# Kernel optimization log

Hardware: AMD Instinct MI355X
Metric: run time of the kernel (lower is better)

The kernel has to match this reference:

```python
import jax, jax.numpy as jnp
import numpy as np

B, D, T = 16384, 1024, 128  # batch, embed_dim, num_degradation_types
V, L = 4, 3                 # variants per sample, degradations per variant


def setup_inputs() -> dict:
    key = jax.random.key(0)
    k1, k2, k3, k4 = jax.random.split(key, 4)
    clean_embeddings = jax.random.normal(k1, (B, D), dtype=jnp.float32)
    W = jax.random.normal(k2, (T, D), dtype=jnp.float32) * (1.0 / np.sqrt(D))
    b = jnp.zeros((T,), dtype=jnp.float32)
    deg_indices = jax.random.randint(k3, (B, V, L), 0, T, dtype=jnp.int32)
    deg_mask = jax.random.randint(k4, (B, V, L), 0, 2, dtype=jnp.int32)
    return {"clean_embeddings": clean_embeddings, "W": W, "b": b,
            "deg_indices": deg_indices, "deg_mask": deg_mask}


def reference(clean_embeddings, W, b, deg_indices, deg_mask):
    # Linear + softmax: [B, T]
    logits = jnp.einsum("bd,td->bt", clean_embeddings, W) + b
    probs = jax.nn.softmax(logits, axis=-1)
    # Gather probs at each (batch, label) pair: [B, V*L] -> [B, V, L]
    flat_idx = deg_indices.reshape(B, V * L)
    gathered = jnp.take_along_axis(probs, flat_idx, axis=1).reshape(B, V, L)
    # Masked sum over all labels of a sample, divided by max(num_variants, 1)=V
    per_sample = (gathered * deg_mask.astype(probs.dtype)).sum(axis=(1, 2)) / V
    return per_sample.sum() / B
```

## Files before the change

### kernel.cpp

```cpp
#include <hip/hip_runtime.h>

#define B_SIZE 16384
#define D_DIM  1024
#define T_DIM  128
#define VLn    12
#define BM     64
#define BKF    64
#define NCHUNK 16
#define NTHR   512
#define GRID   (B_SIZE / BM)
#define ACHB   16384
#define BCHB   16384
#define PAIRB  (ACHB + BCHB)
#define SLSTR  132

typedef _Float16 half8  __attribute__((ext_vector_type(8)));
typedef __fp16   fp16x2 __attribute__((ext_vector_type(2)));
typedef float    f32x4  __attribute__((ext_vector_type(4)));

union Pack16 { fp16x2 h[4]; uint4 u; half8 v; };
union Frag   { uint4 u; half8 h; };

__device__ __forceinline__ uint4 pack8u(float4 v0, float4 v1) {
    Pack16 un;
    un.h[0] = __builtin_amdgcn_cvt_pkrtz(v0.x, v0.y);
    un.h[1] = __builtin_amdgcn_cvt_pkrtz(v0.z, v0.w);
    un.h[2] = __builtin_amdgcn_cvt_pkrtz(v1.x, v1.y);
    un.h[3] = __builtin_amdgcn_cvt_pkrtz(v1.z, v1.w);
    return un.u;
}
__device__ __forceinline__ half8 pack8f(const float* fp) {
    const float2 a = ((const float2*)fp)[0];
    const float2 b = ((const float2*)fp)[1];
    const float2 c = ((const float2*)fp)[2];
    const float2 d = ((const float2*)fp)[3];
    Pack16 un;
    un.h[0] = __builtin_amdgcn_cvt_pkrtz(a.x, a.y);
    un.h[1] = __builtin_amdgcn_cvt_pkrtz(b.x, b.y);
    un.h[2] = __builtin_amdgcn_cvt_pkrtz(c.x, c.y);
    un.h[3] = __builtin_amdgcn_cvt_pkrtz(d.x, d.y);
    return un.v;
}

__device__ __forceinline__ void dma16(const float* g, void* l) {
    __builtin_amdgcn_global_load_lds(
        (const __attribute__((address_space(1))) void*)g,
        (__attribute__((address_space(3))) void*)l, 16, 0, 0);
}

#define WAITV(n) asm volatile("s_waitcnt vmcnt(" #n ")" ::: "memory")
#define SB0()    __builtin_amdgcn_sched_barrier(0)

__global__ __launch_bounds__(256)
void conv_w(const float* __restrict__ W, uint4* __restrict__ Wf,
            float* __restrict__ out) {
    if (blockIdx.x == 0 && threadIdx.x == 0) out[0] = 0.0f;
    const int j    = blockIdx.x * 256 + threadIdx.x;
    const int kc   = j >> 10;
    const int r    = j & 1023;
    const int g    = r >> 6;
    const int lane = r & 63;
    const int n = (g & 7) * 16 + (lane & 15);
    const int k = kc * 64 + (g >> 3) * 32 + ((lane >> 4) << 3);
    const float* src = W + (size_t)n * D_DIM + k;
    Wf[j] = pack8u(*(const float4*)src, *(const float4*)(src + 4));
}

__global__ __launch_bounds__(NTHR, 2)
void qloss_kernel(const float* __restrict__ emb,
                  const uint4* __restrict__ Wf,
                  const float* __restrict__ bias,
                  const int*   __restrict__ didx,
                  const int*   __restrict__ dmsk,
                  float*       __restrict__ out)
{
    __shared__ __align__(16) unsigned char smem[4 * PAIRB + 64];
    float* sL   = (float*)smem;
    float* sRed = (float*)(smem + 4 * PAIRB);

    const int t    = threadIdx.x;
    const int w    = t >> 6;
    const int lane = t & 63;
    const int m15  = lane & 15;
    const int quad = lane >> 4;
    const int r0   = blockIdx.x * BM;

    const int rr = w & 3;
    const int cg = w >> 2;

    const float* aS0 = emb + (size_t)(r0 + 8 * w + quad) * D_DIM
                           + (((m15 * 4) ^ (quad << 3)));
    const float* aS1 = emb + (size_t)(r0 + 8 * w + 4 + quad) * D_DIM
                           + (((m15 * 4) ^ ((4 + quad) << 3)));
    const float* bS = (const float*)(Wf + 2 * w * 64 + lane);

    f32x4 acc[4];
#pragma unroll
    for (int ct = 0; ct < 4; ++ct) acc[ct] = (f32x4){0.f, 0.f, 0.f, 0.f};

    auto issue = [&](int j) {
        unsigned char* Ab = smem + (j & 3) * PAIRB;
        dma16(aS0 + j * BKF, Ab + (8 * w) * 256);
        dma16(aS1 + j * BKF, Ab + (8 * w + 4) * 256);
        unsigned char* Bb = Ab + ACHB;
        dma16(bS + (size_t)j * 4096,        Bb + (2 * w) * 1024);
        dma16(bS + (size_t)j * 4096 + 256,  Bb + (2 * w + 1) * 1024);
    };

    auto compute = [&](int kc) {
        const unsigned char* pb = smem + (kc & 3) * PAIRB;
        const float* Af = (const float*)pb;
        const uint4* Bf = (const uint4*)(pb + ACHB);
#pragma unroll
        for (int st = 0; st < 2; ++st) {
            const int row = 16 * rr + m15;
            const float* fp = Af + row * 64
                            + (((st * 32 + quad * 8) ^ ((m15 & 7) << 3)));
            const half8 a = pack8f(fp);
#pragma unroll
            for (int ct = 0; ct < 4; ++ct) {
                Frag b;
                b.u = Bf[(st * 8 + 4 * cg + ct) * 64 + lane];
                acc[ct] = __builtin_amdgcn_mfma_f32_16x16x32_f16(a, b.h, acc[ct], 0, 0, 0);
            }
        }
    };

    issue(0); issue(1); issue(2);

#pragma unroll
    for (int kc = 0; kc < NCHUNK - 3; ++kc) {
        WAITV(8);
        SB0();
        __builtin_amdgcn_s_barrier();
        SB0();
        issue(kc + 3);
        SB0();
        compute(kc);
    }
    WAITV(8); SB0(); __builtin_amdgcn_s_barrier(); SB0(); compute(13);
    WAITV(4); SB0(); __builtin_amdgcn_s_barrier(); SB0(); compute(14);
    WAITV(0); SB0(); __builtin_amdgcn_s_barrier(); SB0(); compute(15);

    __syncthreads();
    float bv[4];
#pragma unroll
    for (int ct = 0; ct < 4; ++ct) bv[ct] = bias[(4 * cg + ct) * 16 + m15];
#pragma unroll
    for (int i = 0; i < 4; ++i) {
        const int row = 16 * rr + quad * 4 + i;
#pragma unroll
        for (int ct = 0; ct < 4; ++ct)
            sL[row * SLSTR + (4 * cg + ct) * 16 + m15] = acc[ct][i] + bv[ct];
    }
    __syncthreads();

    {
        const int row = t >> 3, sub = t & 7;
        float* base = &sL[row * SLSTR + sub * 16];
        float v[16];
        *(float4*)&v[0]  = *(const float4*)(base);
        *(float4*)&v[4]  = *(const float4*)(base + 4);
        *(float4*)&v[8]  = *(const float4*)(base + 8);
        *(float4*)&v[12] = *(const float4*)(base + 12);
        float m = -1e30f;
#pragma unroll
        for (int j = 0; j < 16; ++j) m = fmaxf(m, v[j]);
#pragma unroll
        for (int off = 1; off < 8; off <<= 1) m = fmaxf(m, __shfl_xor(m, off));
        float ssum = 0.f;
#pragma unroll
        for (int j = 0; j < 16; ++j) { v[j] = __expf(v[j] - m); ssum += v[j]; }
#pragma unroll
        for (int off = 1; off < 8; off <<= 1) ssum += __shfl_xor(ssum, off);
        const float inv = 1.0f / ssum;
#pragma unroll
        for (int j = 0; j < 16; ++j) v[j] *= inv;
        *(float4*)(base)      = *(const float4*)&v[0];
        *(float4*)(base + 4)  = *(const float4*)&v[4];
        *(float4*)(base + 8)  = *(const float4*)&v[8];
        *(float4*)(base + 12) = *(const float4*)&v[12];
    }
    __syncthreads();

    float p = 0.f;
#pragma unroll
    for (int e = 0; e < 2; ++e) {
        const int item = e * 512 + t;
        if (item < BM * VLn) {
            const int gi  = r0 * VLn + item;
            const int row = item / VLn;
            const int mk  = dmsk[gi];
            const int idx = didx[gi];
            if (mk) p += sL[row * SLSTR + idx];
        }
    }
#pragma unroll
    for (int off = 1; off < 64; off <<= 1) p += __shfl_xor(p, off);
    if (lane == 0) sRed[w] = p;
    __syncthreads();
    if (t == 0) {
        float s = 0.f;
#pragma unroll
        for (int i = 0; i < 8; ++i) s += sRed[i];
        atomicAdd(out, s * (1.0f / 65536.0f));
    }
}

extern "C" void kernel_launch(void* const* d_in, const int* in_sizes, int n_in,
                              void* d_out, int out_size, void* d_ws, size_t ws_size,
                              hipStream_t stream) {
    const float* emb  = (const float*)d_in[0];
    const float* W    = (const float*)d_in[1];
    const float* bias = (const float*)d_in[2];
    const int*   didx = (const int*)d_in[3];
    const int*   dmsk = (const int*)d_in[4];
    float* out = (float*)d_out;

    uint4* Wf = (uint4*)d_ws;

    conv_w<<<64, 256, 0, stream>>>(W, Wf, out);
    qloss_kernel<<<GRID, NTHR, 0, stream>>>(emb, Wf, bias, didx, dmsk, out);
}
```

Measured before the change: 114.1 us.

## Load W fragments into registers per wave and drop B staging from LDS

The work split changes so each wave owns 16 output columns across all 64 rows. Its pre-converted W fragments are loaded straight from global memory into registers, prefetched two k-steps ahead, and only the embedding tile goes through LDS via DMA. This removes the B tile from LDS and halves shared memory per block, which could let more blocks fit per CU. In exchange, each wave now reads and converts four A fragments per k-step instead of one, raising LDS read and fp32-to-fp16 conversion work, and the vmcnt wait counts are retuned for the mixed load stream.

```diff
diff --git a/kernel.cpp b/kernel.cpp
--- a/kernel.cpp
+++ b/kernel.cpp
@@ -10,8 +10,7 @@
 #define NTHR   512
 #define GRID   (B_SIZE / BM)
 #define ACHB   16384
-#define BCHB   16384
-#define PAIRB  (ACHB + BCHB)
+#define NSLOT  4
 #define SLSTR  132
 
 typedef _Float16 half8  __attribute__((ext_vector_type(8)));
@@ -74,9 +73,9 @@
                   const int*   __restrict__ dmsk,
                   float*       __restrict__ out)
 {
-    __shared__ __align__(16) unsigned char smem[4 * PAIRB + 64];
+    __shared__ __align__(16) unsigned char smem[NSLOT * ACHB + 64];
     float* sL   = (float*)smem;
-    float* sRed = (float*)(smem + 4 * PAIRB);
+    float* sRed = (float*)(smem + NSLOT * ACHB);
 
     const int t    = threadIdx.x;
     const int w    = t >> 6;
@@ -85,74 +84,76 @@
     const int quad = lane >> 4;
     const int r0   = blockIdx.x * BM;
 
-    const int rr = w & 3;
-    const int cg = w >> 2;
-
     const float* aS0 = emb + (size_t)(r0 + 8 * w + quad) * D_DIM
-                           + (((m15 * 4) ^ (quad << 3)));
+                           + ((m15 * 4) ^ (quad << 3));
     const float* aS1 = emb + (size_t)(r0 + 8 * w + 4 + quad) * D_DIM
-                           + (((m15 * 4) ^ ((4 + quad) << 3)));
-    const float* bS = (const float*)(Wf + 2 * w * 64 + lane);
+                           + ((m15 * 4) ^ ((4 + quad) << 3));
+    const uint4* bP = Wf + lane;
 
     f32x4 acc[4];
 #pragma unroll
-    for (int ct = 0; ct < 4; ++ct) acc[ct] = (f32x4){0.f, 0.f, 0.f, 0.f};
+    for (int rt = 0; rt < 4; ++rt) acc[rt] = (f32x4){0.f, 0.f, 0.f, 0.f};
+
+    Frag bp[4];
+
+#define LOADB(s)                                                              \
+    bp[(s) & 3].u = bP[(size_t)((s) >> 1) * 1024 + (((s) & 1) * 8 + w) * 64]
 
     auto issue = [&](int j) {
-        unsigned char* Ab = smem + (j & 3) * PAIRB;
+        unsigned char* Ab = smem + (j & 3) * ACHB;
         dma16(aS0 + j * BKF, Ab + (8 * w) * 256);
         dma16(aS1 + j * BKF, Ab + (8 * w + 4) * 256);
-        unsigned char* Bb = Ab + ACHB;
-        dma16(bS + (size_t)j * 4096,        Bb + (2 * w) * 1024);
-        dma16(bS + (size_t)j * 4096 + 256,  Bb + (2 * w + 1) * 1024);
     };
 
     auto compute = [&](int kc) {
-        const unsigned char* pb = smem + (kc & 3) * PAIRB;
-        const float* Af = (const float*)pb;
-        const uint4* Bf = (const uint4*)(pb + ACHB);
+        const float* Af = (const float*)(smem + (kc & 3) * ACHB);
 #pragma unroll
         for (int st = 0; st < 2; ++st) {
-            const int row = 16 * rr + m15;
-            const float* fp = Af + row * 64
-                            + (((st * 32 + quad * 8) ^ ((m15 & 7) << 3)));
-            const half8 a = pack8f(fp);
-#pragma unroll
-            for (int ct = 0; ct < 4; ++ct) {
-                Frag b;
-                b.u = Bf[(st * 8 + 4 * cg + ct) * 64 + lane];
-                acc[ct] = __builtin_amdgcn_mfma_f32_16x16x32_f16(a, b.h, acc[ct], 0, 0, 0);
+            const int s = kc * 2 + st;
+            const int ko = (st * 32 + quad * 8);
+#pragma unroll
+            for (int rt = 0; rt < 4; ++rt) {
+                const int row = 16 * rt + m15;
+                const float* fp = Af + row * 64 + (ko ^ ((m15 & 7) << 3));
+                const half8 a = pack8f(fp);
+                acc[rt] = __builtin_amdgcn_mfma_f32_16x16x32_f16(
+                              a, bp[s & 3].h, acc[rt], 0, 0, 0);
             }
         }
     };
 
     issue(0); issue(1); issue(2);
+    LOADB(0); LOADB(1);
 
 #pragma unroll
     for (int kc = 0; kc < NCHUNK - 3; ++kc) {
-        WAITV(8);
+        WAITV(6);
         SB0();
         __builtin_amdgcn_s_barrier();
         SB0();
+        LOADB(2 * kc + 2);
+        LOADB(2 * kc + 3);
         issue(kc + 3);
         SB0();
         compute(kc);
     }
-    WAITV(8); SB0(); __builtin_amdgcn_s_barrier(); SB0(); compute(13);
-    WAITV(4); SB0(); __builtin_amdgcn_s_barrier(); SB0(); compute(14);
-    WAITV(0); SB0(); __builtin_amdgcn_s_barrier(); SB0(); compute(15);
-
-    __syncthreads();
-    float bv[4];
-#pragma unroll
-    for (int ct = 0; ct < 4; ++ct) bv[ct] = bias[(4 * cg + ct) * 16 + m15];
-#pragma unroll
-    for (int i = 0; i < 4; ++i) {
-        const int row = 16 * rr + quad * 4 + i;
-#pragma unroll
-        for (int ct = 0; ct < 4; ++ct)
-            sL[row * SLSTR + (4 * cg + ct) * 16 + m15] = acc[ct][i] + bv[ct];
-    }
+    WAITV(6); SB0(); __builtin_amdgcn_s_barrier(); SB0();
+    LOADB(28); LOADB(29); compute(13);
+    WAITV(4); SB0(); __builtin_amdgcn_s_barrier(); SB0();
+    LOADB(30); LOADB(31); compute(14);
+    WAITV(2); SB0(); __builtin_amdgcn_s_barrier(); SB0();
+    compute(15);
+#undef LOADB
+
+    __syncthreads();
+    const float bv = bias[w * 16 + m15];
+#pragma unroll
+    for (int rt = 0; rt < 4; ++rt)
+#pragma unroll
+        for (int i = 0; i < 4; ++i) {
+            const int row = 16 * rt + quad * 4 + i;
+            sL[row * SLSTR + w * 16 + m15] = acc[rt][i] + bv;
+        }
     __syncthreads();
 
     {
```

Result: no change. 114.2 us (+0.1%).
